# Kernel tuning notes

Hardware: AMD Instinct MI355X
Metric: run time of the kernel (lower is better)

## Reference

```python
import jax, jax.numpy as jnp
import numpy as np

SIZE, D, N, E = 50000, 1024, 50000, 100000


def setup_inputs() -> dict:
    key = jax.random.key(0)
    k1, k2 = jax.random.split(key)
    # torchhd.embeddings.Random produces bipolar {-1,+1} MAP hypervectors
    w = jnp.where(jax.random.uniform(k1, (SIZE, D)) < 0.5, -1.0, 1.0).astype(jnp.float32)
    edge_index = jax.random.randint(k2, (2, E), 0, N, dtype=jnp.int32)
    return {"node_ids_weight": w, "edge_index": edge_index, "num_nodes": N}


def reference(node_ids_weight, edge_index, num_nodes):
    # degree_centrality: in-degree via bincount on columns, normalized
    col = edge_index[1]
    degree = jnp.bincount(col, length=num_nodes)
    pr = degree / num_nodes  # float
    pr_argsort = jnp.argsort(pr)  # stable sort, matches torch sort semantics on ties

    # node_id_hvs[pr_argsort] = weight[:num_nodes]  (scatter assign)
    node_id_hvs = jnp.zeros((num_nodes, node_ids_weight.shape[1]),
                            dtype=node_ids_weight.dtype)
    node_id_hvs = node_id_hvs.at[pr_argsort].set(node_ids_weight[:num_nodes])

    # to_undirected: sort endpoints per edge, then unique columns.
    # jit-friendly unique: lexsort edges, mask out duplicates of the previous edge.
    e = jnp.sort(edge_index, axis=0)  # [2, E], row <= col per edge
    order = jnp.lexsort((e[1], e[0]))
    r = e[0][order]
    c = e[1][order]
    keep = jnp.concatenate([
        jnp.array([True]),
        (r[1:] != r[:-1]) | (c[1:] != c[:-1]),
    ])  # [E] True for first occurrence of each unique edge

    # bind = elementwise multiply of gathered hvs; multiset = sum over edges
    hvs = node_id_hvs[r] * node_id_hvs[c]  # [E, D]
    out = jnp.sum(jnp.where(keep[:, None], hvs, 0.0), axis=0)  # [D]
    return out
```

## Files before the change

kernel.cpp:

```cpp
#include <hip/hip_runtime.h>
#include <stdint.h>

#define DCAP   128
#define CHUNK  1024
#define LOG_TAB 19
#define TAB_SIZE (1u << LOG_TAB)
#define TAB_MASK (TAB_SIZE - 1u)
#define KEMPTY 0xFFFFFFFFu

typedef unsigned int uintv4 __attribute__((ext_vector_type(4)));

__global__ void k_deg_ins(const int* __restrict__ ei, int* __restrict__ degree,
                          unsigned int* __restrict__ tab, int* __restrict__ uA,
                          int* __restrict__ uB, int* __restrict__ count, int E) {
    int e = blockIdx.x * blockDim.x + threadIdx.x;
    if (e >= E) return;
    int a = ei[e], b = ei[E + e];
    atomicAdd(&degree[b], 1);
    int r = min(a, b), c = max(a, b);
    unsigned int key = ((unsigned int)r << 16) | (unsigned int)c;
    unsigned int h = (key * 2654435761u) >> (32 - LOG_TAB);
    for (;;) {
        unsigned int old = atomicCAS(&tab[h], KEMPTY, key);
        if (old == KEMPTY) {
            int idx = atomicAdd(count, 1);
            uA[idx] = r; uB[idx] = c;
            return;
        }
        if (old == key) return;
        h = (h + 1) & TAB_MASK;
    }
}

__global__ __launch_bounds__(CHUNK) void k_chunk_hist(const int* __restrict__ degree,
                                                      int* __restrict__ hist,
                                                      int* __restrict__ chunkHist, int N) {
    __shared__ int sh[DCAP];
    int t = threadIdx.x;
    if (t < DCAP) sh[t] = 0;
    __syncthreads();
    int j = blockIdx.x * CHUNK + t;
    if (j < N) {
        int d = degree[j];
        if (d < DCAP) atomicAdd(&sh[d], 1);
        else          atomicAdd(&hist[d], 1);
    }
    __syncthreads();
    if (t < DCAP) chunkHist[blockIdx.x * DCAP + t] = sh[t];
}

__global__ __launch_bounds__(CHUNK) void k_pos(const int* __restrict__ degree,
                                               const int* __restrict__ chunkHist,
                                               const int* __restrict__ hist,
                                               int* __restrict__ pos,
                                               int N, int E, int numChunks) {
    int t = threadIdx.x;
    if ((int)blockIdx.x < numChunks) {
        __shared__ int sdeg[CHUNK];
        __shared__ int stot[DCAP];
        __shared__ int sbase[DCAP];
        int me = blockIdx.x;
        if (t < DCAP) {
            int tot = 0, pre = 0;
            for (int c = 0; c < numChunks; ++c) {
                int v = chunkHist[c * DCAP + t];
                pre += (c < me) ? v : 0;
                tot += v;
            }
            stot[t] = tot;
            sbase[t] = pre;
        }
        __syncthreads();
        if (t < DCAP) {
            int run = 0;
            for (int d2 = 0; d2 < t; ++d2) run += stot[d2];
            sbase[t] += run;
        }
        int j = me * CHUNK + t;
        int d = (j < N) ? degree[j] : -1;
        sdeg[t] = d;
        __syncthreads();
        if (j < N && d >= 0 && d < DCAP) {
            int r = 0;
            for (int t2 = 0; t2 < t; ++t2) r += (sdeg[t2] == d);
            pos[j] = sbase[d] + r;
        }
    } else {
        int d = DCAP + ((int)blockIdx.x - numChunks) * CHUNK + t;
        if (d > E) return;
        if (hist[d] == 0) return;
        long long suf = 0;
        for (int d2 = d; d2 <= E; ++d2) suf += hist[d2];
        int base = N - (int)suf;
        int cnt = 0;
        for (int j = 0; j < N; ++j)
            if (degree[j] == d) pos[j] = base + cnt++;
    }
}

#define PACK_DEPTH 8
__global__ __launch_bounds__(256) void k_pack_ballot(const float* __restrict__ W,
                                                     uint32_t* __restrict__ Wbits,
                                                     long long G) {
    long long wv0 = ((long long)blockIdx.x * 256 + threadIdx.x) >> 6;
    long long nwv = ((long long)gridDim.x * 256) >> 6;
    int lane = threadIdx.x & 63;
    int k = lane >> 1, half = lane & 1;
    const uintv4* W4 = (const uintv4*)W;
    for (long long gb = wv0 * PACK_DEPTH; gb < G; gb += nwv * PACK_DEPTH) {
        uintv4 u[PACK_DEPTH];
        #pragma unroll
        for (int s = 0; s < PACK_DEPTH; ++s) {
            long long g = gb + s;
            if (g >= G) g = G - 1;
            u[s] = W4[g * 64 + lane];
        }
        #pragma unroll
        for (int s = 0; s < PACK_DEPTH; ++s) {
            long long g = gb + s;
            unsigned long long m0 = __ballot((int)u[s].x < 0);
            unsigned long long m1 = __ballot((int)u[s].y < 0);
            unsigned long long m2 = __ballot((int)u[s].z < 0);
            unsigned long long m3 = __ballot((int)u[s].w < 0);
            if (g < G && lane < 8) {
                unsigned long long m = (k == 0) ? m0 : (k == 1) ? m1
                                     : (k == 2) ? m2 : m3;
                Wbits[g * 8 + lane] = half ? (uint32_t)(m >> 32) : (uint32_t)m;
            }
        }
    }
}

__global__ __launch_bounds__(256) void k_pack_linear(const float* __restrict__ W,
                                                     uint32_t* __restrict__ Wbits, long long NW) {
    long long widx = (long long)blockIdx.x * 256 + threadIdx.x;
    if (widx >= NW) return;
    const uintv4* src = (const uintv4*)(W + widx * 32);
    uint32_t word = 0;
    #pragma unroll
    for (int q = 0; q < 8; ++q) {
        uintv4 u = src[q];
        word |= (u.x >> 31) << (4 * q + 0);
        word |= (u.y >> 31) << (4 * q + 1);
        word |= (u.z >> 31) << (4 * q + 2);
        word |= (u.w >> 31) << (4 * q + 3);
    }
    Wbits[widx] = word;
}

__global__ __launch_bounds__(256) void k_accum_bits(const uint32_t* __restrict__ Wbits,
                                                    const int* __restrict__ pos,
                                                    const int* __restrict__ uA,
                                                    const int* __restrict__ uB,
                                                    const int* __restrict__ count,
                                                    int* __restrict__ neg, int D) {
    __shared__ int sneg[1024];
    int t = threadIdx.x, w = t & 31, slot = t >> 5;
    int wpr = D / 32;
    for (int i = t; i < D; i += 256) sneg[i] = 0;
    __syncthreads();
    int cnt = *count;
    int cnts[32];
    #pragma unroll
    for (int d = 0; d < 32; ++d) cnts[d] = 0;
    if (w < wpr) {
        for (int base = blockIdx.x * 8; base < cnt; base += gridDim.x * 8) {
            int e = base + slot;
            if (e < cnt) {
                size_t ra = (size_t)pos[uA[e]] * wpr;
                size_t rb = (size_t)pos[uB[e]] * wpr;
                uint32_t x = Wbits[ra + w] ^ Wbits[rb + w];
                #pragma unroll
                for (int d = 0; d < 32; ++d) cnts[d] += (x >> d) & 1u;
            }
        }
        #pragma unroll
        for (int d = 0; d < 32; ++d) atomicAdd(&sneg[w * 32 + d], cnts[d]);
    }
    __syncthreads();
    for (int i = t; i < D; i += 256)
        if (sneg[i]) atomicAdd(&neg[i], sneg[i]);
}

__global__ void k_finalize(const int* __restrict__ neg, const int* __restrict__ count,
                           float* __restrict__ out, int D, int permuted) {
    int d = blockIdx.x * blockDim.x + threadIdx.x;
    if (d >= D) return;
    int ni;
    if (permuted) {
        int off = d & 255, q = d >> 8;
        int k = off & 3, l = off >> 2, half = l >> 5, b = l & 31;
        ni = (q * 8 + 2 * k + half) * 32 + b;
    } else {
        ni = d;
    }
    out[d] = (float)(*count - 2 * neg[ni]);
}

static inline size_t align256(size_t x) { return (x + 255) & ~(size_t)255; }

extern "C" void kernel_launch(void* const* d_in, const int* in_sizes, int n_in,
                              void* d_out, int out_size, void* d_ws, size_t ws_size,
                              hipStream_t stream) {
    const float* W  = (const float*)d_in[0];
    const int*   ei = (const int*)d_in[1];
    const int D = out_size;
    const int N = in_sizes[0] / D;
    const int E = in_sizes[1] / 2;
    const int numChunks = (N + CHUNK - 1) / CHUNK;
    const long long ND = (long long)N * D;
    const long long NW = ND / 32;
    const long long G  = ND / 256;

    char* p = (char*)d_ws;
    char* zbase = p;
    int* degree       = (int*)p;          p += align256((size_t)N * 4);
    int* hist         = (int*)p;          p += align256((size_t)(E + 1) * 4);
    int* count        = (int*)p;          p += 256;
    int* neg          = (int*)p;          p += align256((size_t)D * 4);
    size_t zbytes = (size_t)(p - zbase);
    int* chunkHist    = (int*)p;          p += align256((size_t)numChunks * DCAP * 4);
    int* pos          = (int*)p;          p += align256((size_t)N * 4);
    unsigned int* tab = (unsigned int*)p; p += (size_t)TAB_SIZE * 4;
    int* uA           = (int*)p;          p += align256((size_t)E * 4);
    int* uB           = (int*)p;          p += align256((size_t)E * 4);
    uint32_t* Wbits   = (uint32_t*)p;     p += align256((size_t)NW * 4);

    hipMemsetAsync(zbase, 0, zbytes, stream);
    hipMemsetAsync(tab, 0xFF, (size_t)TAB_SIZE * 4, stream);

    k_deg_ins<<<(E + 255) / 256, 256, 0, stream>>>(ei, degree, tab, uA, uB, count, E);
    k_chunk_hist<<<numChunks, CHUNK, 0, stream>>>(degree, hist, chunkHist, N);
    int nLargeBlocks = (E + 1 - DCAP + CHUNK - 1) / CHUNK;
    k_pos<<<numChunks + nLargeBlocks, CHUNK, 0, stream>>>(degree, chunkHist, hist,
                                                          pos, N, E, numChunks);

    int permuted = (D % 256 == 0);
    if (permuted) {
        k_pack_ballot<<<2048, 256, 0, stream>>>(W, Wbits, G);
    } else {
        k_pack_linear<<<(int)((NW + 255) / 256), 256, 0, stream>>>(W, Wbits, NW);
    }

    k_accum_bits<<<2048, 256, 0, stream>>>(Wbits, pos, uA, uB, count, neg, D);
    k_finalize<<<(D + 255) / 256, 256, 0, stream>>>(neg, count, (float*)d_out, D, permuted);
}
```

Baseline: 145.0 us.

## Fuse graph preprocessing and weight packing into one persistent kernel with grid barriers

Merges edge insertion, degree histogram, rank computation and the ballot-based weight packing into a single kernel. The first 64 blocks run the sequential graph phases, separated by software grid barriers, while every block also packs the weights, so the bandwidth-bound packing overlaps the latency-bound graph work and several launches go away. It also halves the hash table size and cuts the accumulation grid from 2048 to 512 blocks. The spin barriers depend on all 64 chain blocks being co-resident, which the occupancy-based grid sizing is meant to ensure. The large-degree fallback is now a slow serial scan over only 64 blocks.

```diff
diff --git a/kernel.cpp b/kernel.cpp
--- a/kernel.cpp
+++ b/kernel.cpp
@@ -3,12 +3,173 @@
 
 #define DCAP   128
 #define CHUNK  1024
-#define LOG_TAB 19
+#define LOG_TAB 18
 #define TAB_SIZE (1u << LOG_TAB)
 #define TAB_MASK (TAB_SIZE - 1u)
 #define KEMPTY 0xFFFFFFFFu
+#define NCHAIN 64
 
 typedef unsigned int uintv4 __attribute__((ext_vector_type(4)));
+
+__device__ __forceinline__ int aload(int* p) { return atomicAdd(p, 0); }
+
+__device__ __forceinline__ void cbar(int* bar, int* gen, int phase) {
+    __syncthreads();
+    if (threadIdx.x == 0) {
+        atomicAdd(bar, 1);
+        if (blockIdx.x == 0) {
+            while (atomicAdd(bar, 0) < NCHAIN * phase) __builtin_amdgcn_s_sleep(2);
+            atomicExch(gen, phase);
+        } else {
+            while (atomicAdd(gen, 0) < phase) __builtin_amdgcn_s_sleep(2);
+        }
+    }
+    __syncthreads();
+}
+
+#define PACK_DEPTH 8
+__device__ __forceinline__ void packAll(const float* __restrict__ W,
+                                        uint32_t* __restrict__ Wbits,
+                                        long long G, int NB) {
+    long long wv0 = ((long long)blockIdx.x * 256 + threadIdx.x) >> 6;
+    long long nwv = ((long long)NB * 256) >> 6;
+    int lane = threadIdx.x & 63;
+    int k = lane >> 1, half = lane & 1;
+    const uintv4* W4 = (const uintv4*)W;
+    for (long long gb = wv0 * PACK_DEPTH; gb < G; gb += nwv * PACK_DEPTH) {
+        uintv4 u[PACK_DEPTH];
+        #pragma unroll
+        for (int s = 0; s < PACK_DEPTH; ++s) {
+            long long g = gb + s;
+            if (g >= G) g = G - 1;
+            u[s] = W4[g * 64 + lane];
+        }
+        #pragma unroll
+        for (int s = 0; s < PACK_DEPTH; ++s) {
+            long long g = gb + s;
+            unsigned long long m0 = __ballot((int)u[s].x < 0);
+            unsigned long long m1 = __ballot((int)u[s].y < 0);
+            unsigned long long m2 = __ballot((int)u[s].z < 0);
+            unsigned long long m3 = __ballot((int)u[s].w < 0);
+            if (g < G && lane < 8) {
+                unsigned long long m = (k == 0) ? m0 : (k == 1) ? m1
+                                     : (k == 2) ? m2 : m3;
+                Wbits[g * 8 + lane] = half ? (uint32_t)(m >> 32) : (uint32_t)m;
+            }
+        }
+    }
+}
+
+__global__ __launch_bounds__(256) void k_fused(
+    const float* __restrict__ W, const int* __restrict__ ei,
+    int* degree, int* hist, int* chunkHist, int* pos,
+    unsigned int* tab, int* uA, int* uB, int* count,
+    uint32_t* Wbits, int* bar, int* gen,
+    int N, int E, long long G, int numChunks, int NB)
+{
+    if ((int)blockIdx.x < NCHAIN) {
+        __shared__ int sdeg[CHUNK];
+        __shared__ int stot[DCAP];
+        __shared__ int sbase[DCAP];
+        __shared__ int sh[DCAP];
+        const int tid = threadIdx.x;
+
+        for (int e = blockIdx.x * 256 + tid; e < E; e += NCHAIN * 256) {
+            int a = ei[e], b = ei[E + e];
+            atomicAdd(&degree[b], 1);
+            int r = min(a, b), c = max(a, b);
+            unsigned int key = ((unsigned int)r << 16) | (unsigned int)c;
+            unsigned int h = (key * 2654435761u) >> (32 - LOG_TAB);
+            for (;;) {
+                unsigned int old = atomicCAS(&tab[h], KEMPTY, key);
+                if (old == KEMPTY) { int i2 = atomicAdd(count, 1); uA[i2] = r; uB[i2] = c; break; }
+                if (old == key) break;
+                h = (h + 1) & TAB_MASK;
+            }
+        }
+        cbar(bar, gen, 1);
+
+        for (int c = blockIdx.x; c < numChunks; c += NCHAIN) {
+            if (tid < DCAP) sh[tid] = 0;
+            __syncthreads();
+            for (int q = 0; q < CHUNK / 256; ++q) {
+                int j = c * CHUNK + q * 256 + tid;
+                if (j < N) {
+                    int d = aload(&degree[j]);
+                    if (d < DCAP) atomicAdd(&sh[d], 1);
+                    else          atomicAdd(&hist[d], 1);
+                }
+            }
+            __syncthreads();
+            if (tid < DCAP) atomicExch(&chunkHist[c * DCAP + tid], sh[tid]);
+            __syncthreads();
+        }
+        cbar(bar, gen, 2);
+
+        for (int c = blockIdx.x; c < numChunks; c += NCHAIN) {
+            if (tid < DCAP) {
+                int tot = 0, pre = 0;
+                for (int c2 = 0; c2 < numChunks; ++c2) {
+                    int v = aload(&chunkHist[c2 * DCAP + tid]);
+                    pre += (c2 < c) ? v : 0;
+                    tot += v;
+                }
+                stot[tid] = tot;
+                sbase[tid] = pre;
+            }
+            __syncthreads();
+            if (tid < DCAP) {
+                int run = 0;
+                for (int d2 = 0; d2 < tid; ++d2) run += stot[d2];
+                sbase[tid] += run;
+            }
+            for (int q = 0; q < CHUNK / 256; ++q) {
+                int j = c * CHUNK + q * 256 + tid;
+                sdeg[q * 256 + tid] = (j < N) ? aload(&degree[j]) : -1;
+            }
+            __syncthreads();
+            for (int q = 0; q < CHUNK / 256; ++q) {
+                int idx = q * 256 + tid;
+                int j = c * CHUNK + idx;
+                int d = sdeg[idx];
+                if (j < N && d >= 0 && d < DCAP) {
+                    int r = 0;
+                    for (int t2 = 0; t2 < idx; ++t2) r += (sdeg[t2] == d);
+                    pos[j] = sbase[d] + r;
+                }
+            }
+            __syncthreads();
+        }
+        for (int d = DCAP + blockIdx.x * 256 + tid; d <= E; d += NCHAIN * 256) {
+            if (aload(&hist[d]) != 0) {
+                long long suf = 0;
+                for (int d2 = d; d2 <= E; ++d2) suf += aload(&hist[d2]);
+                int base = N - (int)suf;
+                int cnt2 = 0;
+                for (int j = 0; j < N; ++j)
+                    if (aload(&degree[j]) == d) { pos[j] = base + cnt2; ++cnt2; }
+            }
+        }
+    }
+    packAll(W, Wbits, G, NB);
+}
+
+__global__ __launch_bounds__(256) void k_pack_linear(const float* __restrict__ W,
+                                                     uint32_t* __restrict__ Wbits, long long NW) {
+    long long widx = (long long)blockIdx.x * 256 + threadIdx.x;
+    if (widx >= NW) return;
+    const uintv4* src = (const uintv4*)(W + widx * 32);
+    uint32_t word = 0;
+    #pragma unroll
+    for (int q = 0; q < 8; ++q) {
+        uintv4 u = src[q];
+        word |= (u.x >> 31) << (4 * q + 0);
+        word |= (u.y >> 31) << (4 * q + 1);
+        word |= (u.z >> 31) << (4 * q + 2);
+        word |= (u.w >> 31) << (4 * q + 3);
+    }
+    Wbits[widx] = word;
+}
 
 __global__ void k_deg_ins(const int* __restrict__ ei, int* __restrict__ degree,
                           unsigned int* __restrict__ tab, int* __restrict__ uA,
@@ -22,16 +183,11 @@
     unsigned int h = (key * 2654435761u) >> (32 - LOG_TAB);
     for (;;) {
         unsigned int old = atomicCAS(&tab[h], KEMPTY, key);
-        if (old == KEMPTY) {
-            int idx = atomicAdd(count, 1);
-            uA[idx] = r; uB[idx] = c;
-            return;
-        }
+        if (old == KEMPTY) { int idx = atomicAdd(count, 1); uA[idx] = r; uB[idx] = c; return; }
         if (old == key) return;
         h = (h + 1) & TAB_MASK;
     }
 }
-
 __global__ __launch_bounds__(CHUNK) void k_chunk_hist(const int* __restrict__ degree,
                                                       int* __restrict__ hist,
                                                       int* __restrict__ chunkHist, int N) {
@@ -48,7 +204,6 @@
     __syncthreads();
     if (t < DCAP) chunkHist[blockIdx.x * DCAP + t] = sh[t];
 }
-
 __global__ __launch_bounds__(CHUNK) void k_pos(const int* __restrict__ degree,
                                                const int* __restrict__ chunkHist,
                                                const int* __restrict__ hist,
@@ -98,56 +253,6 @@
     }
 }
 
-#define PACK_DEPTH 8
-__global__ __launch_bounds__(256) void k_pack_ballot(const float* __restrict__ W,
-                                                     uint32_t* __restrict__ Wbits,
-                                                     long long G) {
-    long long wv0 = ((long long)blockIdx.x * 256 + threadIdx.x) >> 6;
-    long long nwv = ((long long)gridDim.x * 256) >> 6;
-    int lane = threadIdx.x & 63;
-    int k = lane >> 1, half = lane & 1;
-    const uintv4* W4 = (const uintv4*)W;
-    for (long long gb = wv0 * PACK_DEPTH; gb < G; gb += nwv * PACK_DEPTH) {
-        uintv4 u[PACK_DEPTH];
-        #pragma unroll
-        for (int s = 0; s < PACK_DEPTH; ++s) {
-            long long g = gb + s;
-            if (g >= G) g = G - 1;
-            u[s] = W4[g * 64 + lane];
-        }
-        #pragma unroll
-        for (int s = 0; s < PACK_DEPTH; ++s) {
-            long long g = gb + s;
-            unsigned long long m0 = __ballot((int)u[s].x < 0);
-            unsigned long long m1 = __ballot((int)u[s].y < 0);
-            unsigned long long m2 = __ballot((int)u[s].z < 0);
-            unsigned long long m3 = __ballot((int)u[s].w < 0);
-            if (g < G && lane < 8) {
-                unsigned long long m = (k == 0) ? m0 : (k == 1) ? m1
-                                     : (k == 2) ? m2 : m3;
-                Wbits[g * 8 + lane] = half ? (uint32_t)(m >> 32) : (uint32_t)m;
-            }
-        }
-    }
-}
-
-__global__ __launch_bounds__(256) void k_pack_linear(const float* __restrict__ W,
-                                                     uint32_t* __restrict__ Wbits, long long NW) {
-    long long widx = (long long)blockIdx.x * 256 + threadIdx.x;
-    if (widx >= NW) return;
-    const uintv4* src = (const uintv4*)(W + widx * 32);
-    uint32_t word = 0;
-    #pragma unroll
-    for (int q = 0; q < 8; ++q) {
-        uintv4 u = src[q];
-        word |= (u.x >> 31) << (4 * q + 0);
-        word |= (u.y >> 31) << (4 * q + 1);
-        word |= (u.z >> 31) << (4 * q + 2);
-        word |= (u.w >> 31) << (4 * q + 3);
-    }
-    Wbits[widx] = word;
-}
-
 __global__ __launch_bounds__(256) void k_accum_bits(const uint32_t* __restrict__ Wbits,
                                                     const int* __restrict__ pos,
                                                     const int* __restrict__ uA,
@@ -214,6 +319,8 @@
 
     char* p = (char*)d_ws;
     char* zbase = p;
+    int* bar          = (int*)p;          p += 256;
+    int* gen          = (int*)p;          p += 256;
     int* degree       = (int*)p;          p += align256((size_t)N * 4);
     int* hist         = (int*)p;          p += align256((size_t)(E + 1) * 4);
     int* count        = (int*)p;          p += 256;
@@ -229,19 +336,36 @@
     hipMemsetAsync(zbase, 0, zbytes, stream);
     hipMemsetAsync(tab, 0xFF, (size_t)TAB_SIZE * 4, stream);
 
-    k_deg_ins<<<(E + 255) / 256, 256, 0, stream>>>(ei, degree, tab, uA, uB, count, E);
-    k_chunk_hist<<<numChunks, CHUNK, 0, stream>>>(degree, hist, chunkHist, N);
-    int nLargeBlocks = (E + 1 - DCAP + CHUNK - 1) / CHUNK;
-    k_pos<<<numChunks + nLargeBlocks, CHUNK, 0, stream>>>(degree, chunkHist, hist,
-                                                          pos, N, E, numChunks);
-
+    int dev = 0;
+    hipGetDevice(&dev);
+    int cus = 0;
+    hipDeviceGetAttribute(&cus, hipDeviceAttributeMultiprocessorCount, dev);
+    int maxB = 0;
+    hipOccupancyMaxActiveBlocksPerMultiprocessor(&maxB, k_fused, 256, 0);
+    int NB = cus * maxB;
+    if (NB > 2048) NB = 2048;
+
+    bool fused = (D % 256 == 0) && (NB >= NCHAIN * 2);
     int permuted = (D % 256 == 0);
-    if (permuted) {
-        k_pack_ballot<<<2048, 256, 0, stream>>>(W, Wbits, G);
+
+    if (fused) {
+        k_fused<<<NB, 256, 0, stream>>>(W, ei, degree, hist, chunkHist, pos,
+                                        tab, uA, uB, count, Wbits, bar, gen,
+                                        N, E, G, numChunks, NB);
     } else {
-        k_pack_linear<<<(int)((NW + 255) / 256), 256, 0, stream>>>(W, Wbits, NW);
-    }
-
-    k_accum_bits<<<2048, 256, 0, stream>>>(Wbits, pos, uA, uB, count, neg, D);
+        k_deg_ins<<<(E + 255) / 256, 256, 0, stream>>>(ei, degree, tab, uA, uB, count, E);
+        k_chunk_hist<<<numChunks, CHUNK, 0, stream>>>(degree, hist, chunkHist, N);
+        int nLB = (E + 1 - DCAP + CHUNK - 1) / CHUNK;
+        k_pos<<<numChunks + nLB, CHUNK, 0, stream>>>(degree, chunkHist, hist, pos,
+                                                     N, E, numChunks);
+        if (permuted) {
+            k_pack_linear<<<(int)((NW + 255) / 256), 256, 0, stream>>>(W, Wbits, NW);
+            permuted = 0;
+        } else {
+            k_pack_linear<<<(int)((NW + 255) / 256), 256, 0, stream>>>(W, Wbits, NW);
+        }
+    }
+
+    k_accum_bits<<<512, 256, 0, stream>>>(Wbits, pos, uA, uB, count, neg, D);
     k_finalize<<<(D + 255) / 256, 256, 0, stream>>>(neg, count, (float*)d_out, D, permuted);
 }
```

Measured after the change: 189.5 us. 1.31x slower.
